# Kernel tuning notes

Measured on AMD Instinct MI355X. Metric: run time of the kernel, lower is better.

The kernel has to match this reference:

```python
import jax, jax.numpy as jnp
import numpy as np

NUM_HEADS = 8
DIM_V = 128
LN_EPS = 1e-5


def _ln(x, g, b):
    m = jnp.mean(x, axis=-1, keepdims=True)
    v = jnp.var(x, axis=-1, keepdims=True)
    return (x - m) * jax.lax.rsqrt(v + LN_EPS) * g + b


def _gcn(x, adj_norm, W, b):
    # DenseGCNConv: out = D^-1/2 (A+I) D^-1/2 (x W) + b
    return jnp.einsum('bnm,bmf->bnf', adj_norm, x @ W) + b


def setup_inputs() -> dict:
    key = jax.random.key(0)
    ks = jax.random.split(key, 24)
    B, N, D = 8, 1024, 128
    Hd = NUM_HEADS * DIM_V  # 1024
    s = lambda fan: 1.0 / np.sqrt(fan)
    inp = {
        'H': jax.random.normal(ks[0], (B, N, D), jnp.float32),
        'A': jax.random.uniform(ks[1], (B, N, N), jnp.float32),
        'W_Q': jax.random.normal(ks[2], (D, Hd), jnp.float32) * s(D),
        'b_Q': jnp.zeros((Hd,), jnp.float32),
        'W_K': jax.random.normal(ks[3], (D, Hd), jnp.float32) * s(D),
        'b_K': jnp.zeros((Hd,), jnp.float32),
        'W_V': jax.random.normal(ks[4], (D, Hd), jnp.float32) * s(D),
        'b_V': jnp.zeros((Hd,), jnp.float32),
        'B_bias': jax.random.normal(ks[5], (NUM_HEADS, N, N), jnp.float32) * 0.02,
        'W_O': jax.random.normal(ks[6], (Hd, D), jnp.float32) * s(Hd),
        'g0': jnp.ones((D,), jnp.float32), 'be0': jnp.zeros((D,), jnp.float32),
        'g1': jnp.ones((D,), jnp.float32), 'be1': jnp.zeros((D,), jnp.float32),
        'g2': jnp.ones((D,), jnp.float32), 'be2': jnp.zeros((D,), jnp.float32),
        'g3': jnp.ones((D,), jnp.float32), 'be3': jnp.zeros((D,), jnp.float32),
        'W1': jax.random.normal(ks[7], (D, D), jnp.float32) * s(D),
        'b1': jnp.zeros((D,), jnp.float32),
        'W2': jax.random.normal(ks[8], (D, D), jnp.float32) * s(D),
        'b2': jnp.zeros((D,), jnp.float32),
    }
    return inp


def reference(H, A, W_Q, b_Q, W_K, b_K, W_V, b_V, B_bias, W_O,
              g0, be0, g1, be1, g2, be2, g3, be3, W1, b1, W2, b2):
    B, N, D = H.shape
    dk_scale = 1.0 / np.sqrt(np.float32(D))  # sqrt(dim_K)

    residual = H
    Hn = _ln(H, g0, be0)  # norm_type 'sw': pre-norm

    # GCN adjacency normalization with self-loops (shared by Q/K/V layers)
    I = jnp.eye(N, dtype=A.dtype)
    Ahat = A * (1.0 - I) + I
    dis = jax.lax.rsqrt(jnp.maximum(Ahat.sum(-1), 1.0))  # [B,N]
    adj_norm = dis[:, :, None] * Ahat * dis[:, None, :]

    Q = _gcn(Hn, adj_norm, W_Q, b_Q)  # [B,N,H*dV]
    K = _gcn(Hn, adj_norm, W_K, b_K)
    V = _gcn(Hn, adj_norm, W_V, b_V)

    # split heads: feature slice h*dV:(h+1)*dV -> head h
    Q_ = Q.reshape(B, N, NUM_HEADS, DIM_V).transpose(0, 2, 1, 3)
    K_ = K.reshape(B, N, NUM_HEADS, DIM_V).transpose(0, 2, 1, 3)
    V_ = V.reshape(B, N, NUM_HEADS, DIM_V).transpose(0, 2, 1, 3)

    scores = jnp.einsum('bhnd,bhmd->bhnm', Q_, K_) * dk_scale
    scores = scores + B_bias[None]  # 'BL': blended with learned per-head bias
    attn = jax.nn.softmax(scores, axis=-1)
    MH = jnp.einsum('bhnm,bhmd->bhnd', attn, V_)  # [B,H,N,dV]

    MH = _ln(MH, g1, be1)  # 'sw' GN1

    # concat heads back to features
    MHc = MH.transpose(0, 2, 1, 3).reshape(B, N, NUM_HEADS * DIM_V)
    O = MHc @ W_O + residual
    O = _ln(O, g2, be2)

    RO = jax.nn.relu(jax.nn.relu(O @ W1 + b1) @ W2 + b2)
    RO = _ln(RO, g3, be3)  # 'sw' GN3
    return O + RO
```

## Files before the change

### kernel.cpp

```cpp
#include <hip/hip_runtime.h>
#include <hip/hip_bf16.h>
#include <stdint.h>

typedef __attribute__((ext_vector_type(8))) short bf16x8;
typedef __attribute__((ext_vector_type(4))) short s16x4;
typedef __attribute__((ext_vector_type(4))) float f32x4;

__device__ __forceinline__ float bf2f(short s) {
    union { float f; uint32_t u; } v; v.u = ((uint32_t)(uint16_t)s) << 16; return v.f;
}
__device__ __forceinline__ short f2bf(float f) {
    union { float f; uint32_t u; } v; v.f = f;
    uint32_t u = v.u;
    u += 0x7FFFu + ((u >> 16) & 1u);
    return (short)(u >> 16);
}
__device__ __forceinline__ void gload_lds16(const void* g, void* l) {
    __builtin_amdgcn_global_load_lds(
        (const __attribute__((address_space(1))) uint32_t*)g,
        (__attribute__((address_space(3))) uint32_t*)l, 16, 0, 0);
}

template<int MODE>
__global__ __launch_bounds__(256) void ln_kernel(
    const float* __restrict__ x, const float* __restrict__ res,
    const float* __restrict__ gamma, const float* __restrict__ beta,
    float* __restrict__ outf, short* __restrict__ outb)
{
    const int row = blockIdx.x * 4 + (threadIdx.x >> 6);
    const int lane = threadIdx.x & 63;
    const long base = (long)row * 128;
    float2 v;
    if (MODE == 1) {
        v.x = 0.f; v.y = 0.f;
#pragma unroll
        for (int p = 0; p < 2; ++p) {
            float2 t = *(const float2*)(x + (long)p * 1048576 + base + lane * 2);
            v.x += t.x; v.y += t.y;
        }
        float2 rr = *(const float2*)(res + base + lane * 2);
        v.x += rr.x; v.y += rr.y;
    } else {
        v = *(const float2*)(x + base + lane * 2);
    }
    float s = v.x + v.y, s2 = v.x * v.x + v.y * v.y;
#pragma unroll
    for (int o = 32; o; o >>= 1) { s += __shfl_xor(s, o); s2 += __shfl_xor(s2, o); }
    const float mean = s * (1.f / 128.f);
    const float var = s2 * (1.f / 128.f) - mean * mean;
    const float rs = rsqrtf(var + 1e-5f);
    const float y0 = (v.x - mean) * rs * gamma[lane * 2] + beta[lane * 2];
    const float y1 = (v.y - mean) * rs * gamma[lane * 2 + 1] + beta[lane * 2 + 1];
    if (MODE == 0 || MODE == 1) {
        uint32_t pk = (uint32_t)(uint16_t)f2bf(y0) | ((uint32_t)(uint16_t)f2bf(y1) << 16);
        *(uint32_t*)(outb + base + lane * 2) = pk;
    }
    if (MODE == 1) {
        float2 o2; o2.x = y0; o2.y = y1;
        *(float2*)(outf + base + lane * 2) = o2;
    }
    if (MODE == 2) {
        float2 rr = *(const float2*)(res + base + lane * 2);
        float2 o2; o2.x = y0 + rr.x; o2.y = y1 + rr.y;
        *(float2*)(outf + base + lane * 2) = o2;
    }
}

__global__ __launch_bounds__(256) void prep1_kernel(
    const float* __restrict__ H, const float* __restrict__ A, const float* __restrict__ Bb,
    const float* __restrict__ WQ, const float* __restrict__ WK, const float* __restrict__ WV,
    const float* __restrict__ bQ, const float* __restrict__ bK, const float* __restrict__ bV,
    const float* __restrict__ WO, const float* __restrict__ W1, const float* __restrict__ W2,
    const float* __restrict__ g0, const float* __restrict__ be0,
    short* __restrict__ Hn, float* __restrict__ dis, short* __restrict__ biasb,
    short* __restrict__ WqkvT, float* __restrict__ bqkv, short* __restrict__ WoT,
    short* __restrict__ W1T, short* __restrict__ W2T)
{
    __shared__ float red[4];
    const int id = blockIdx.x;
    const int tid = threadIdx.x;
    if (id < 2048) {
        const int row = id * 4 + (tid >> 6);
        const int lane = tid & 63;
        const long base = (long)row * 128;
        float2 v = *(const float2*)(H + base + lane * 2);
        float s = v.x + v.y, s2 = v.x * v.x + v.y * v.y;
#pragma unroll
        for (int o = 32; o; o >>= 1) { s += __shfl_xor(s, o); s2 += __shfl_xor(s2, o); }
        const float mean = s * (1.f / 128.f);
        const float var = s2 * (1.f / 128.f) - mean * mean;
        const float rs = rsqrtf(var + 1e-5f);
        const float y0 = (v.x - mean) * rs * g0[lane * 2] + be0[lane * 2];
        const float y1 = (v.y - mean) * rs * g0[lane * 2 + 1] + be0[lane * 2 + 1];
        uint32_t pk = (uint32_t)(uint16_t)f2bf(y0) | ((uint32_t)(uint16_t)f2bf(y1) << 16);
        *(uint32_t*)(Hn + base + lane * 2) = pk;
    } else if (id < 10240) {
        const int bn = id - 2048;
        const int n = bn & 1023;
        float4 v = ((const float4*)(A + (long)bn * 1024))[tid];
        float s = v.x + v.y + v.z + v.w;
        if ((n >> 2) == tid) {
            s += 1.f - ((const float*)&v)[n & 3];
        }
#pragma unroll
        for (int o = 32; o; o >>= 1) s += __shfl_xor(s, o);
        if ((tid & 63) == 0) red[tid >> 6] = s;
        __syncthreads();
        if (tid == 0) {
            float t = red[0] + red[1] + red[2] + red[3];
            dis[bn] = rsqrtf(fmaxf(t, 1.f));
        }
    } else if (id < 18432) {
        const long i = ((long)(id - 10240) * 256 + tid) * 4;
        float4 v = *(const float4*)(Bb + i);
        s16x4 o; o[0] = f2bf(v.x); o[1] = f2bf(v.y); o[2] = f2bf(v.z); o[3] = f2bf(v.w);
        *(s16x4*)(biasb + i) = o;
    } else {
        const int gid = (id - 18432) * 256 + tid;
        if (gid < 393216) {
            const int f = gid >> 7, k = gid & 127;
            const float* W = (f < 1024) ? WQ : (f < 2048 ? WK : WV);
            WqkvT[gid] = f2bf(W[k * 1024 + (f & 1023)]);
        } else if (gid < 396288) {
            const int f = gid - 393216;
            const float* bb = (f < 1024) ? bQ : (f < 2048 ? bK : bV);
            bqkv[f] = bb[f & 1023];
        } else if (gid < 527360) {
            const int t = gid - 396288;
            const int j = t >> 10, i = t & 1023;
            WoT[t] = f2bf(WO[i * 128 + j]);
        } else if (gid < 543744) {
            const int t = gid - 527360;
            W1T[t] = f2bf(W1[(t & 127) * 128 + (t >> 7)]);
        } else if (gid < 560128) {
            const int t = gid - 543744;
            W2T[t] = f2bf(W2[(t & 127) * 128 + (t >> 7)]);
        }
    }
}

__global__ __launch_bounds__(256) void prep2_kernel(
    const float* __restrict__ A, const float* __restrict__ dis, const short* __restrict__ Hn,
    short* __restrict__ adj, short* __restrict__ HnT)
{
    __shared__ short T[64][72];
    const int id = blockIdx.x;
    const int tid = threadIdx.x;
    if (id < 8192) {
        const int bn = id;
        const int b = bn >> 10, n = bn & 1023;
        const float dn = dis[bn];
        float4 v = ((const float4*)(A + (long)bn * 1024))[tid];
        const int m0 = tid * 4;
        const float* dm = dis + b * 1024 + m0;
        s16x4 o;
#pragma unroll
        for (int j = 0; j < 4; ++j) {
            float av = (m0 + j == n) ? 1.f : ((const float*)&v)[j];
            o[j] = f2bf(av * dn * dm[j]);
        }
        *(s16x4*)(adj + (long)bn * 1024 + m0) = o;
    } else {
        const int t = id - 8192;
        const int bx = t & 15, by = (t >> 4) & 1, bz = t >> 5;
        const int m0 = bx * 64, f0 = by * 64;
        const int row = tid >> 2;
        const int c = (tid & 3) * 16;
        const short* src = Hn + (long)(bz * 1024 + m0 + row) * 128 + f0 + c;
        *(bf16x8*)&T[row][c] = *(const bf16x8*)src;
        *(bf16x8*)&T[row][c + 8] = *(const bf16x8*)(src + 8);
        __syncthreads();
        short* dst = HnT + ((long)bz * 128 + f0 + row) * 1024 + m0 + c;
        bf16x8 o0, o1;
#pragma unroll
        for (int i = 0; i < 8; ++i) { o0[i] = T[c + i][row]; o1[i] = T[c + 8 + i][row]; }
        *(bf16x8*)dst = o0;
        *(bf16x8*)(dst + 8) = o1;
    }
}

__global__ __launch_bounds__(256) void ahred_kernel(const float* __restrict__ AHp, short* __restrict__ AH)
{
    const long i = ((long)blockIdx.x * 256 + threadIdx.x) * 4;
    const int b = (int)(i >> 17);
    const long r = i & 131071;
    const float* p = AHp + (long)b * 262144 + r;
    float4 v0 = *(const float4*)p;
    float4 v1 = *(const float4*)(p + 131072);
    s16x4 o;
    o[0] = f2bf(v0.x + v1.x);
    o[1] = f2bf(v0.y + v1.y);
    o[2] = f2bf(v0.z + v1.z);
    o[3] = f2bf(v0.w + v1.w);
    *(s16x4*)(AH + i) = o;
}

__global__ __launch_bounds__(256) void vtrans_kernel(const short* __restrict__ QKV, short* __restrict__ VT)
{
    const int bh = blockIdx.z, b = bh >> 3, h = bh & 7;
    const int n0 = blockIdx.x * 64, d0 = blockIdx.y * 64;
    __shared__ short T[64][72];
    const int row = threadIdx.x >> 2;
    const int c = (threadIdx.x & 3) * 16;
    const short* src = QKV + (long)(b * 1024 + n0 + row) * 3072 + 2048 + h * 128 + d0 + c;
    *(bf16x8*)&T[row][c] = *(const bf16x8*)src;
    *(bf16x8*)&T[row][c + 8] = *(const bf16x8*)(src + 8);
    __syncthreads();
    short* dst = VT + (long)(bh * 128 + d0 + row) * 1024 + n0 + c;
    bf16x8 o0, o1;
#pragma unroll
    for (int i = 0; i < 8; ++i) { o0[i] = T[c + i][row]; o1[i] = T[c + 8 + i][row]; }
    *(bf16x8*)dst = o0;
    *(bf16x8*)(dst + 8) = o1;
}

template<int BIAS_MODE, bool RELU, bool OUT_BF16>
__global__ __launch_bounds__(256) void gemm_kernel(
    const short* __restrict__ A, const short* __restrict__ Bt,
    const float* __restrict__ bias, void* __restrict__ Cv,
    int K, int lda, int ldb, int ldc,
    long batchA, long batchB, long batchC)
{
    __shared__ __align__(16) short Asm[128 * 32];
    __shared__ __align__(16) short Bsm[128 * 32];
    const int tid = threadIdx.x, lane = tid & 63, wave = tid >> 6;
    const int li = lane & 15, g = lane >> 4;
    const int mt = blockIdx.y * 128, nt = blockIdx.x * 128;
    A += (long)blockIdx.z * batchA;
    Bt += (long)blockIdx.z * batchB;

    const int wr = (wave >> 1) * 64, wc = (wave & 1) * 64;
    f32x4 acc[4][4] = {};

    const int srow = lane >> 2;
    const int scol = (lane & 3) * 8;
    const long aoff0 = (long)(mt + wave * 32 + srow) * lda + scol;
    const long aoff1 = aoff0 + (long)16 * lda;
    const long boff0 = (long)(nt + wave * 32 + srow) * ldb + scol;
    const long boff1 = boff0 + (long)16 * ldb;
    short* ad0 = &Asm[wave * 1024];
    short* ad1 = &Asm[wave * 1024 + 512];
    short* bd0 = &Bsm[wave * 1024];
    short* bd1 = &Bsm[wave * 1024 + 512];

    for (int k0 = 0; k0 < K; k0 += 32) {
        gload_lds16(A + aoff0 + k0, ad0);
        gload_lds16(A + aoff1 + k0, ad1);
        gload_lds16(Bt + boff0 + k0, bd0);
        gload_lds16(Bt + boff1 + k0, bd1);
        __syncthreads();
        bf16x8 af[4], bf[4];
#pragma unroll
        for (int m = 0; m < 4; ++m) af[m] = *(const bf16x8*)&Asm[(wr + m * 16 + li) * 32 + g * 8];
#pragma unroll
        for (int n = 0; n < 4; ++n) bf[n] = *(const bf16x8*)&Bsm[(wc + n * 16 + li) * 32 + g * 8];
#pragma unroll
        for (int m = 0; m < 4; ++m)
#pragma unroll
            for (int n = 0; n < 4; ++n)
                acc[m][n] = __builtin_amdgcn_mfma_f32_16x16x32_bf16(af[m], bf[n], acc[m][n], 0, 0, 0);
        __syncthreads();
    }

    const long cbase = (long)blockIdx.z * batchC;
#pragma unroll
    for (int m = 0; m < 4; ++m) {
        const int row0 = mt + wr + m * 16 + g * 4;
#pragma unroll
        for (int n = 0; n < 4; ++n) {
            const int col = nt + wc + n * 16 + li;
            float bc = (BIAS_MODE == 1) ? bias[col] : 0.f;
#pragma unroll
            for (int r = 0; r < 4; ++r) {
                float x = acc[m][n][r] + bc;
                if (RELU) x = fmaxf(x, 0.f);
                const long idx = cbase + (long)(row0 + r) * ldc + col;
                if (OUT_BF16) ((short*)Cv)[idx] = f2bf(x);
                else          ((float*)Cv)[idx] = x;
            }
        }
    }
}

template<int BIAS_MODE, bool RELU, bool OUT_BF16, int KSPLIT = 1>
__global__ __launch_bounds__(256) void gemm64_kernel(
    const short* __restrict__ A, const short* __restrict__ Bt,
    const float* __restrict__ bias, void* __restrict__ Cv,
    int K, int lda, int ldb, int ldc,
    long batchA, long batchB, long batchC)
{
    __shared__ __align__(16) short Asm[64 * 32];
    __shared__ __align__(16) short Bsm[64 * 32];
    const int tid = threadIdx.x, lane = tid & 63, wave = tid >> 6;
    const int li = lane & 15, g = lane >> 4;
    const int mt = blockIdx.y * 64, nt = blockIdx.x * 64;
    const int wr = (wave >> 1) * 32, wc = (wave & 1) * 32;
    const int zb = blockIdx.z / KSPLIT;
    const int kc = blockIdx.z % KSPLIT;
    A += (long)zb * batchA + (long)kc * K;
    Bt += (long)zb * batchB + (long)kc * K;
    f32x4 acc[2][2] = {};

    const int srow = lane >> 2;
    const int scol = (lane & 3) * 8;
    const long aoff = (long)(mt + wave * 16 + srow) * lda + scol;
    const long boff = (long)(nt + wave * 16 + srow) * ldb + scol;

    for (int k0 = 0; k0 < K; k0 += 32) {
        gload_lds16(A + aoff + k0, &Asm[wave * 512]);
        gload_lds16(Bt + boff + k0, &Bsm[wave * 512]);
        __syncthreads();
        bf16x8 af[2], bf[2];
#pragma unroll
        for (int m = 0; m < 2; ++m) af[m] = *(const bf16x8*)&Asm[(wr + m * 16 + li) * 32 + g * 8];
#pragma unroll
        for (int n = 0; n < 2; ++n) bf[n] = *(const bf16x8*)&Bsm[(wc + n * 16 + li) * 32 + g * 8];
#pragma unroll
        for (int m = 0; m < 2; ++m)
#pragma unroll
            for (int n = 0; n < 2; ++n)
                acc[m][n] = __builtin_amdgcn_mfma_f32_16x16x32_bf16(af[m], bf[n], acc[m][n], 0, 0, 0);
        __syncthreads();
    }

    const long cbase = (long)blockIdx.z * batchC;
#pragma unroll
    for (int m = 0; m < 2; ++m) {
        const int row0 = mt + wr + m * 16 + g * 4;
#pragma unroll
        for (int n = 0; n < 2; ++n) {
            const int col = nt + wc + n * 16 + li;
            float bc = (BIAS_MODE == 1) ? bias[col] : 0.f;
#pragma unroll
            for (int r = 0; r < 4; ++r) {
                float x = acc[m][n][r] + bc;
                if (RELU) x = fmaxf(x, 0.f);
                const long idx = cbase + (long)(row0 + r) * ldc + col;
                if (OUT_BF16) ((short*)Cv)[idx] = f2bf(x);
                else          ((float*)Cv)[idx] = x;
            }
        }
    }
}

__global__ __launch_bounds__(512, 2) void attn_kernel(
    const short* __restrict__ QKV, const short* __restrict__ VT,
    const short* __restrict__ biasb,
    const float* __restrict__ g1v, const float* __restrict__ be1v,
    short* __restrict__ MHc)
{
    const int tid = threadIdx.x;
    const int lane = tid & 63;
    const int wave = tid >> 6;
    const int li = lane & 15;
    const int g = lane >> 4;

    const int id = blockIdx.x;
    const int h = id & 7;
    const int b = (id >> 3) & 7;
    const int qt = id >> 6;
    const int q0 = qt * 128;

    __shared__ __align__(16) short Ksm[64 * 128];
    __shared__ __align__(16) short Vsm[128 * 64];
    __shared__ __align__(16) short Psm[8][16 * 72];

    bf16x8 qf[4];
    {
        const short* Qb = QKV + ((long)(b * 1024 + q0 + wave * 16 + li) * 3072 + h * 128);
#pragma unroll
        for (int dc = 0; dc < 4; ++dc)
            qf[dc] = *(const bf16x8*)(Qb + dc * 32 + g * 8);
    }

    float ll[4];
#pragma unroll
    for (int r = 0; r < 4; ++r) ll[r] = 0.f;
    f32x4 oacc[8] = {};

    const long kbase = (long)(b * 1024) * 3072 + 1024 + h * 128;
    const int kr0 = wave * 8 + g;
    const int kc0 = ((li * 16) ^ ((kr0 & 7) << 4)) >> 1;
    const int kc1 = ((li * 16) ^ (((kr0 + 4) & 7) << 4)) >> 1;
    const int vd_loc = lane >> 3;
    const int vcol = (((lane & 7) * 16) ^ (vd_loc << 4)) >> 1;
    const long vrowbase = ((long)(b * 8 + h) * 128) * 1024;

    const float scale = 0.08838834764831845f;
    const long bb_row0 = (long)h * 1024 + q0 + wave * 16 + g * 4;

    for (int kv0 = 0; kv0 < 1024; kv0 += 64) {
        gload_lds16(QKV + kbase + (long)(kv0 + kr0) * 3072 + kc0, &Ksm[wave * 1024]);
        gload_lds16(QKV + kbase + (long)(kv0 + kr0 + 4) * 3072 + kc1, &Ksm[wave * 1024 + 512]);
        gload_lds16(VT + vrowbase + (long)(wave * 16 + vd_loc) * 1024 + kv0 + vcol,
                    &Vsm[(wave * 16) * 64]);
        gload_lds16(VT + vrowbase + (long)(wave * 16 + 8 + vd_loc) * 1024 + kv0 + vcol,
                    &Vsm[(wave * 16 + 8) * 64]);
        __syncthreads();

        float bs[4][4];
#pragma unroll
        for (int r = 0; r < 4; ++r) {
            const short* bp = biasb + (bb_row0 + r) * 1024 + kv0 + li;
#pragma unroll
            for (int j = 0; j < 4; ++j)
                bs[r][j] = bf2f(bp[j * 16]);
        }

        const f32x4 fz = {0.f, 0.f, 0.f, 0.f};
        f32x4 sacc[4] = {fz, fz, fz, fz};
#pragma unroll
        for (int j = 0; j < 4; ++j) {
            const int r = j * 16 + li;
            const int sw = (r & 7) << 4;
#pragma unroll
            for (int dc = 0; dc < 4; ++dc) {
                bf16x8 kf = *(const bf16x8*)((const char*)Ksm + r * 256 + ((dc * 64 + g * 16) ^ sw));
                sacc[j] = __builtin_amdgcn_mfma_f32_16x16x32_bf16(qf[dc], kf, sacc[j], 0, 0, 0);
            }
        }

#pragma unroll
        for (int r = 0; r < 4; ++r) {
            short* pp = &Psm[wave][(g * 4 + r) * 72];
            float psum = 0.f;
#pragma unroll
            for (int j = 0; j < 4; ++j) {
                const float p = __expf(sacc[j][r] * scale + bs[r][j]);
                psum += p;
                pp[j * 16 + li] = f2bf(p);
            }
            ll[r] += psum;
        }

#pragma unroll
        for (int c = 0; c < 2; ++c) {
            bf16x8 pf = *(const bf16x8*)((const char*)&Psm[wave][0] + li * 144 + c * 64 + g * 16);
#pragma unroll
            for (int df = 0; df < 8; ++df) {
                bf16x8 vf = *(const bf16x8*)((const char*)Vsm + (df * 16 + li) * 128
                                             + ((c * 64 + g * 16) ^ ((li & 7) << 4)));
                oacc[df] = __builtin_amdgcn_mfma_f32_16x16x32_bf16(pf, vf, oacc[df], 0, 0, 0);
            }
        }
        __syncthreads();
    }

#pragma unroll
    for (int r = 0; r < 4; ++r) {
        const int qloc = g * 4 + r;
        float l = ll[r];
#pragma unroll
        for (int o = 1; o < 16; o <<= 1) l += __shfl_xor(l, o);
        const float inv = 1.f / l;
        float vals[8];
        float s1 = 0.f, s2 = 0.f;
#pragma unroll
        for (int df = 0; df < 8; ++df) {
            float v = oacc[df][r] * inv;
            vals[df] = v; s1 += v; s2 += v * v;
        }
#pragma unroll
        for (int o = 1; o < 16; o <<= 1) { s1 += __shfl_xor(s1, o); s2 += __shfl_xor(s2, o); }
        const float mean = s1 * (1.f / 128.f);
        const float var = s2 * (1.f / 128.f) - mean * mean;
        const float rs = rsqrtf(var + 1e-5f);
        const long orow = (long)(b * 1024 + q0 + wave * 16 + qloc) * 1024 + h * 128;
#pragma unroll
        for (int df = 0; df < 8; ++df) {
            const int d = df * 16 + li;
            MHc[orow + d] = f2bf((vals[df] - mean) * rs * g1v[d] + be1v[d]);
        }
    }
}

extern "C" void kernel_launch(void* const* d_in, const int* in_sizes, int n_in,
                              void* d_out, int out_size, void* d_ws, size_t ws_size,
                              hipStream_t stream)
{
    const float* H  = (const float*)d_in[0];
    const float* A  = (const float*)d_in[1];
    const float* WQ = (const float*)d_in[2];
    const float* bQ = (const float*)d_in[3];
    const float* WK = (const float*)d_in[4];
    const float* bK = (const float*)d_in[5];
    const float* WV = (const float*)d_in[6];
    const float* bV = (const float*)d_in[7];
    const float* Bb = (const float*)d_in[8];
    const float* WO = (const float*)d_in[9];
    const float* g0 = (const float*)d_in[10]; const float* be0 = (const float*)d_in[11];
    const float* g1 = (const float*)d_in[12]; const float* be1 = (const float*)d_in[13];
    const float* g2 = (const float*)d_in[14]; const float* be2 = (const float*)d_in[15];
    const float* g3 = (const float*)d_in[16]; const float* be3 = (const float*)d_in[17];
    const float* W1 = (const float*)d_in[18]; const float* b1 = (const float*)d_in[19];
    const float* W2 = (const float*)d_in[20]; const float* b2 = (const float*)d_in[21];
    float* out = (float*)d_out;

    char* ws = (char*)d_ws;
    short* Hn    = (short*)(ws + 0);
    short* adj   = (short*)(ws + 2097152);
    float* dis   = (float*)(ws + 18874368);
    short* WqkvT = (short*)(ws + 18907136);
    float* bqkv  = (float*)(ws + 19693568);
    short* WoT   = (short*)(ws + 19705856);
    short* W1T   = (short*)(ws + 19968000);
    short* W2T   = (short*)(ws + 20000768);
    short* biasb = (short*)(ws + 20033536);
    short* QKV   = (short*)(ws + 36810752);
    float* AHp   = (float*)(ws + 87142400);
    short* AH    = (short*)(ws + 103919616);
    short* HnT   = (short*)(ws + 106016768);
    short* VT    = adj;
    short* MHc   = (short*)(ws + 87142400);
    float* preO4 = (float*)(ws + 36810752);
    float* O     = (float*)(ws + 108113920);
    short* Obf   = (short*)(ws + 112308224);
    short* G1    = (short*)(ws + 114405376);
    float* G2    = (float*)(ws + 116502528);

    prep1_kernel<<<20620, 256, 0, stream>>>(H, A, Bb, WQ, WK, WV, bQ, bK, bV,
                                            WO, W1, W2, g0, be0,
                                            Hn, dis, biasb, WqkvT, bqkv, WoT, W1T, W2T);
    prep2_kernel<<<8448, 256, 0, stream>>>(A, dis, Hn, adj, HnT);

    gemm64_kernel<0, false, false, 2><<<dim3(2, 16, 16), 256, 0, stream>>>(
        adj, HnT, nullptr, AHp, 512, 1024, 1024, 128,
        1048576L, 131072L, 131072L);
    ahred_kernel<<<1024, 256, 0, stream>>>(AHp, AH);

    gemm_kernel<1, false, true><<<dim3(24, 64, 1), 256, 0, stream>>>(
        AH, WqkvT, bqkv, QKV, 128, 128, 128, 3072, 0, 0, 0);

    vtrans_kernel<<<dim3(16, 2, 64), 256, 0, stream>>>(QKV, VT);
    attn_kernel<<<512, 512, 0, stream>>>(QKV, VT, biasb, g1, be1, MHc);

    gemm64_kernel<0, false, false, 2><<<dim3(2, 128, 2), 256, 0, stream>>>(
        MHc, WoT, nullptr, preO4, 512, 1024, 1024, 128, 0, 0, 1048576L);
    ln_kernel<1><<<2048, 256, 0, stream>>>(preO4, H, g2, be2, O, Obf);
    gemm64_kernel<1, true, true><<<dim3(2, 128, 1), 256, 0, stream>>>(
        Obf, W1T, b1, G1, 128, 128, 128, 128, 0, 0, 0);
    gemm64_kernel<1, true, false><<<dim3(2, 128, 1), 256, 0, stream>>>(
        G1, W2T, b2, G2, 128, 128, 128, 128, 0, 0, 0);
    ln_kernel<2><<<2048, 256, 0, stream>>>(G2, O, g3, be3, out, nullptr);
}
```

Before: 163.6 us.

## Split attention over two KV halves with separate combine and LayerNorm kernel

The attention kernel now runs on a 2-D grid where each block handles half of the key/value range. Each block writes unnormalized partial outputs in bf16 plus its partial softmax denominators. A new combine kernel sums the two partials, normalizes them and applies the GN1 LayerNorm. The bias is also prescaled by log2(e) during prep, so the inner loop can use exp2f with a folded scale instead of __expf. The split is meant to double the number of attention blocks for better CU occupancy and tail balance, at the cost of extra partial-output traffic and an additional kernel launch.

After: 184.7 us. 1.13x slower.

```diff
diff --git a/kernel.cpp b/kernel.cpp
--- a/kernel.cpp
+++ b/kernel.cpp
@@ -51,11 +51,9 @@
     const float rs = rsqrtf(var + 1e-5f);
     const float y0 = (v.x - mean) * rs * gamma[lane * 2] + beta[lane * 2];
     const float y1 = (v.y - mean) * rs * gamma[lane * 2 + 1] + beta[lane * 2 + 1];
-    if (MODE == 0 || MODE == 1) {
+    if (MODE == 1) {
         uint32_t pk = (uint32_t)(uint16_t)f2bf(y0) | ((uint32_t)(uint16_t)f2bf(y1) << 16);
         *(uint32_t*)(outb + base + lane * 2) = pk;
-    }
-    if (MODE == 1) {
         float2 o2; o2.x = y0; o2.y = y1;
         *(float2*)(outf + base + lane * 2) = o2;
     }
@@ -111,9 +109,11 @@
             dis[bn] = rsqrtf(fmaxf(t, 1.f));
         }
     } else if (id < 18432) {
+        const float l2e = 1.4426950408889634f;
         const long i = ((long)(id - 10240) * 256 + tid) * 4;
         float4 v = *(const float4*)(Bb + i);
-        s16x4 o; o[0] = f2bf(v.x); o[1] = f2bf(v.y); o[2] = f2bf(v.z); o[3] = f2bf(v.w);
+        s16x4 o; o[0] = f2bf(v.x * l2e); o[1] = f2bf(v.y * l2e);
+        o[2] = f2bf(v.z * l2e); o[3] = f2bf(v.w * l2e);
         *(s16x4*)(biasb + i) = o;
     } else {
         const int gid = (id - 18432) * 256 + tid;
@@ -346,8 +346,7 @@
 __global__ __launch_bounds__(512, 2) void attn_kernel(
     const short* __restrict__ QKV, const short* __restrict__ VT,
     const short* __restrict__ biasb,
-    const float* __restrict__ g1v, const float* __restrict__ be1v,
-    short* __restrict__ MHc)
+    short* __restrict__ Opart, float* __restrict__ llpart)
 {
     const int tid = threadIdx.x;
     const int lane = tid & 63;
@@ -360,6 +359,8 @@
     const int b = (id >> 3) & 7;
     const int qt = id >> 6;
     const int q0 = qt * 128;
+    const int kvh = blockIdx.y;
+    const int kvbeg = kvh << 9;
 
     __shared__ __align__(16) short Ksm[64 * 128];
     __shared__ __align__(16) short Vsm[128 * 64];
@@ -386,10 +387,10 @@
     const int vcol = (((lane & 7) * 16) ^ (vd_loc << 4)) >> 1;
     const long vrowbase = ((long)(b * 8 + h) * 128) * 1024;
 
-    const float scale = 0.08838834764831845f;
+    const float scale2 = 0.12753102f;
     const long bb_row0 = (long)h * 1024 + q0 + wave * 16 + g * 4;
 
-    for (int kv0 = 0; kv0 < 1024; kv0 += 64) {
+    for (int kv0 = kvbeg; kv0 < kvbeg + 512; kv0 += 64) {
         gload_lds16(QKV + kbase + (long)(kv0 + kr0) * 3072 + kc0, &Ksm[wave * 1024]);
         gload_lds16(QKV + kbase + (long)(kv0 + kr0 + 4) * 3072 + kc1, &Ksm[wave * 1024 + 512]);
         gload_lds16(VT + vrowbase + (long)(wave * 16 + vd_loc) * 1024 + kv0 + vcol,
@@ -426,7 +427,7 @@
             float psum = 0.f;
 #pragma unroll
             for (int j = 0; j < 4; ++j) {
-                const float p = __expf(sacc[j][r] * scale + bs[r][j]);
+                const float p = exp2f(sacc[j][r] * scale2 + bs[r][j]);
                 psum += p;
                 pp[j * 16 + li] = f2bf(p);
             }
@@ -452,26 +453,47 @@
         float l = ll[r];
 #pragma unroll
         for (int o = 1; o < 16; o <<= 1) l += __shfl_xor(l, o);
-        const float inv = 1.f / l;
-        float vals[8];
-        float s1 = 0.f, s2 = 0.f;
-#pragma unroll
-        for (int df = 0; df < 8; ++df) {
-            float v = oacc[df][r] * inv;
-            vals[df] = v; s1 += v; s2 += v * v;
-        }
-#pragma unroll
-        for (int o = 1; o < 16; o <<= 1) { s1 += __shfl_xor(s1, o); s2 += __shfl_xor(s2, o); }
-        const float mean = s1 * (1.f / 128.f);
-        const float var = s2 * (1.f / 128.f) - mean * mean;
-        const float rs = rsqrtf(var + 1e-5f);
-        const long orow = (long)(b * 1024 + q0 + wave * 16 + qloc) * 1024 + h * 128;
-#pragma unroll
-        for (int df = 0; df < 8; ++df) {
-            const int d = df * 16 + li;
-            MHc[orow + d] = f2bf((vals[df] - mean) * rs * g1v[d] + be1v[d]);
-        }
-    }
+        const int q = q0 + wave * 16 + qloc;
+        if (li == 0)
+            llpart[((long)(kvh * 8 + b) * 8 + h) * 1024 + q] = l;
+        const long orow = (long)kvh * 8388608 + (long)(b * 1024 + q) * 1024 + h * 128;
+#pragma unroll
+        for (int df = 0; df < 8; ++df)
+            Opart[orow + df * 16 + li] = f2bf(oacc[df][r]);
+    }
+}
+
+__global__ __launch_bounds__(256) void attncomb_kernel(
+    const short* __restrict__ Opart, const float* __restrict__ llpart,
+    const float* __restrict__ g1v, const float* __restrict__ be1v,
+    short* __restrict__ MHc)
+{
+    const int unit = blockIdx.x * 4 + (threadIdx.x >> 6);
+    const int lane = threadIdx.x & 63;
+    const int h = unit & 7;
+    const int rowg = unit >> 3;
+    const int b = rowg >> 10;
+    const long lidx = ((long)b * 8 + h) * 1024 + (rowg & 1023);
+    const float l = llpart[lidx] + llpart[65536 + lidx];
+    const float inv = 1.f / l;
+
+    const long base = (long)rowg * 1024 + h * 128 + lane * 2;
+    uint32_t u0 = *(const uint32_t*)(Opart + base);
+    uint32_t u1 = *(const uint32_t*)(Opart + 8388608 + base);
+    const float x0 = (bf2f((short)(u0 & 0xFFFF)) + bf2f((short)(u1 & 0xFFFF))) * inv;
+    const float x1 = (bf2f((short)(u0 >> 16)) + bf2f((short)(u1 >> 16))) * inv;
+
+    float s = x0 + x1, s2 = x0 * x0 + x1 * x1;
+#pragma unroll
+    for (int o = 32; o; o >>= 1) { s += __shfl_xor(s, o); s2 += __shfl_xor(s2, o); }
+    const float mean = s * (1.f / 128.f);
+    const float var = s2 * (1.f / 128.f) - mean * mean;
+    const float rs = rsqrtf(var + 1e-5f);
+    const int d = lane * 2;
+    const float y0 = (x0 - mean) * rs * g1v[d] + be1v[d];
+    const float y1 = (x1 - mean) * rs * g1v[d + 1] + be1v[d + 1];
+    uint32_t pk = (uint32_t)(uint16_t)f2bf(y0) | ((uint32_t)(uint16_t)f2bf(y1) << 16);
+    *(uint32_t*)(MHc + base) = pk;
 }
 
 extern "C" void kernel_launch(void* const* d_in, const int* in_sizes, int n_in,
@@ -511,7 +533,9 @@
     short* AH    = (short*)(ws + 103919616);
     short* HnT   = (short*)(ws + 106016768);
     short* VT    = adj;
-    short* MHc   = (short*)(ws + 87142400);
+    short* Opart = (short*)(ws + 87142400);
+    float* llpart= (float*)(ws + 18874368);
+    short* MHc   = (short*)(ws + 2097152);
     float* preO4 = (float*)(ws + 36810752);
     float* O     = (float*)(ws + 108113920);
     short* Obf   = (short*)(ws + 112308224);
@@ -532,7 +556,9 @@
         AH, WqkvT, bqkv, QKV, 128, 128, 128, 3072, 0, 0, 0);
 
     vtrans_kernel<<<dim3(16, 2, 64), 256, 0, stream>>>(QKV, VT);
-    attn_kernel<<<512, 512, 0, stream>>>(QKV, VT, biasb, g1, be1, MHc);
+
+    attn_kernel<<<dim3(512, 2), 512, 0, stream>>>(QKV, VT, biasb, Opart, llpart);
+    attncomb_kernel<<<16384, 256, 0, stream>>>(Opart, llpart, g1, be1, MHc);
 
     gemm64_kernel<0, false, false, 2><<<dim3(2, 128, 2), 256, 0, stream>>>(
         MHc, WoT, nullptr, preO4, 512, 1024, 1024, 128, 0, 0, 1048576L);
```

## Fuse V transpose into QKV GEMM epilogue and switch softmax to exp2

Applied to the files above, without the earlier changes.

The QKV projection GEMM now writes the V columns straight into the transposed per-head VT layout in its epilogue, which removes the separate vtrans kernel launch and its extra read and write of V. The attention softmax uses exp2f with a log2(e)-folded scale, and the bf16 bias is prescaled by log2(e) in prep, which saves a multiply per exponent. The epilogue for V now does strided 8-byte stores instead of coalesced row stores. The unused MODE 0 path in the LayerNorm kernel is also trimmed.

Result: slower. 175.6 us (+7.3%).

```diff
diff --git a/kernel.cpp b/kernel.cpp
--- a/kernel.cpp
+++ b/kernel.cpp
@@ -51,11 +51,9 @@
     const float rs = rsqrtf(var + 1e-5f);
     const float y0 = (v.x - mean) * rs * gamma[lane * 2] + beta[lane * 2];
     const float y1 = (v.y - mean) * rs * gamma[lane * 2 + 1] + beta[lane * 2 + 1];
-    if (MODE == 0 || MODE == 1) {
+    if (MODE == 1) {
         uint32_t pk = (uint32_t)(uint16_t)f2bf(y0) | ((uint32_t)(uint16_t)f2bf(y1) << 16);
         *(uint32_t*)(outb + base + lane * 2) = pk;
-    }
-    if (MODE == 1) {
         float2 o2; o2.x = y0; o2.y = y1;
         *(float2*)(outf + base + lane * 2) = o2;
     }
@@ -111,9 +109,11 @@
             dis[bn] = rsqrtf(fmaxf(t, 1.f));
         }
     } else if (id < 18432) {
+        const float l2e = 1.4426950408889634f;
         const long i = ((long)(id - 10240) * 256 + tid) * 4;
         float4 v = *(const float4*)(Bb + i);
-        s16x4 o; o[0] = f2bf(v.x); o[1] = f2bf(v.y); o[2] = f2bf(v.z); o[3] = f2bf(v.w);
+        s16x4 o; o[0] = f2bf(v.x * l2e); o[1] = f2bf(v.y * l2e);
+        o[2] = f2bf(v.z * l2e); o[3] = f2bf(v.w * l2e);
         *(s16x4*)(biasb + i) = o;
     } else {
         const int gid = (id - 18432) * 256 + tid;
@@ -195,31 +195,12 @@
     *(s16x4*)(AH + i) = o;
 }
 
-__global__ __launch_bounds__(256) void vtrans_kernel(const short* __restrict__ QKV, short* __restrict__ VT)
-{
-    const int bh = blockIdx.z, b = bh >> 3, h = bh & 7;
-    const int n0 = blockIdx.x * 64, d0 = blockIdx.y * 64;
-    __shared__ short T[64][72];
-    const int row = threadIdx.x >> 2;
-    const int c = (threadIdx.x & 3) * 16;
-    const short* src = QKV + (long)(b * 1024 + n0 + row) * 3072 + 2048 + h * 128 + d0 + c;
-    *(bf16x8*)&T[row][c] = *(const bf16x8*)src;
-    *(bf16x8*)&T[row][c + 8] = *(const bf16x8*)(src + 8);
-    __syncthreads();
-    short* dst = VT + (long)(bh * 128 + d0 + row) * 1024 + n0 + c;
-    bf16x8 o0, o1;
-#pragma unroll
-    for (int i = 0; i < 8; ++i) { o0[i] = T[c + i][row]; o1[i] = T[c + 8 + i][row]; }
-    *(bf16x8*)dst = o0;
-    *(bf16x8*)(dst + 8) = o1;
-}
-
-template<int BIAS_MODE, bool RELU, bool OUT_BF16>
+template<int BIAS_MODE, bool RELU, bool OUT_BF16, bool VTOUT = false>
 __global__ __launch_bounds__(256) void gemm_kernel(
     const short* __restrict__ A, const short* __restrict__ Bt,
     const float* __restrict__ bias, void* __restrict__ Cv,
     int K, int lda, int ldb, int ldc,
-    long batchA, long batchB, long batchC)
+    long batchA, long batchB, long batchC, short* __restrict__ VTp = nullptr)
 {
     __shared__ __align__(16) short Asm[128 * 32];
     __shared__ __align__(16) short Bsm[128 * 32];
@@ -270,13 +251,26 @@
         for (int n = 0; n < 4; ++n) {
             const int col = nt + wc + n * 16 + li;
             float bc = (BIAS_MODE == 1) ? bias[col] : 0.f;
-#pragma unroll
-            for (int r = 0; r < 4; ++r) {
-                float x = acc[m][n][r] + bc;
-                if (RELU) x = fmaxf(x, 0.f);
-                const long idx = cbase + (long)(row0 + r) * ldc + col;
-                if (OUT_BF16) ((short*)Cv)[idx] = f2bf(x);
-                else          ((float*)Cv)[idx] = x;
+            if (VTOUT && col >= 2048) {
+                const int d = col & 127;
+                const int h = (col >> 7) & 7;
+                s16x4 o4;
+#pragma unroll
+                for (int r = 0; r < 4; ++r) {
+                    float x = acc[m][n][r] + bc;
+                    o4[r] = f2bf(x);
+                }
+                short* dst = VTp + ((long)((row0 >> 10) * 8 + h) * 128 + d) * 1024 + (row0 & 1023);
+                *(s16x4*)dst = o4;
+            } else {
+#pragma unroll
+                for (int r = 0; r < 4; ++r) {
+                    float x = acc[m][n][r] + bc;
+                    if (RELU) x = fmaxf(x, 0.f);
+                    const long idx = cbase + (long)(row0 + r) * ldc + col;
+                    if (OUT_BF16) ((short*)Cv)[idx] = f2bf(x);
+                    else          ((float*)Cv)[idx] = x;
+                }
             }
         }
     }
@@ -386,7 +380,7 @@
     const int vcol = (((lane & 7) * 16) ^ (vd_loc << 4)) >> 1;
     const long vrowbase = ((long)(b * 8 + h) * 128) * 1024;
 
-    const float scale = 0.08838834764831845f;
+    const float scale2 = 0.12753102f;
     const long bb_row0 = (long)h * 1024 + q0 + wave * 16 + g * 4;
 
     for (int kv0 = 0; kv0 < 1024; kv0 += 64) {
@@ -426,7 +420,7 @@
             float psum = 0.f;
 #pragma unroll
             for (int j = 0; j < 4; ++j) {
-                const float p = __expf(sacc[j][r] * scale + bs[r][j]);
+                const float p = exp2f(sacc[j][r] * scale2 + bs[r][j]);
                 psum += p;
                 pp[j * 16 + li] = f2bf(p);
             }
@@ -528,10 +522,9 @@
         1048576L, 131072L, 131072L);
     ahred_kernel<<<1024, 256, 0, stream>>>(AHp, AH);
 
-    gemm_kernel<1, false, true><<<dim3(24, 64, 1), 256, 0, stream>>>(
-        AH, WqkvT, bqkv, QKV, 128, 128, 128, 3072, 0, 0, 0);
-
-    vtrans_kernel<<<dim3(16, 2, 64), 256, 0, stream>>>(QKV, VT);
+    gemm_kernel<1, false, true, true><<<dim3(24, 64, 1), 256, 0, stream>>>(
+        AH, WqkvT, bqkv, QKV, 128, 128, 128, 3072, 0, 0, 0, VT);
+
     attn_kernel<<<512, 512, 0, stream>>>(QKV, VT, biasb, g1, be1, MHc);
 
     gemm64_kernel<0, false, false, 2><<<dim3(2, 128, 2), 256, 0, stream>>>(
```

## Fuse adjacency normalization into the A·Hn GEMM and drop the bf16 adj buffer

Applied to the files above, without the earlier changes.

Instead of writing a normalized bf16 adjacency matrix (16 MB) in prep2 and reading it back in a generic GEMM, a new ahgemm kernel loads raw fp32 A, applies the self-loop and D^-1/2 scaling in registers, converts to bf16 and stores it to LDS before the MFMA. This removes one full write and one full read of the adjacency. In exchange, the fp32 A read doubles the A-side bytes per tile, and the new kernel is single-buffered with a synchronous register load path, so latency hiding may be worse than in the previous GEMM. The MODE==0 LN branch is also trimmed.

After: 171.6 us, median of 2. 1.05x slower.

```diff
diff --git a/kernel.cpp b/kernel.cpp
--- a/kernel.cpp
+++ b/kernel.cpp
@@ -51,11 +51,9 @@
     const float rs = rsqrtf(var + 1e-5f);
     const float y0 = (v.x - mean) * rs * gamma[lane * 2] + beta[lane * 2];
     const float y1 = (v.y - mean) * rs * gamma[lane * 2 + 1] + beta[lane * 2 + 1];
-    if (MODE == 0 || MODE == 1) {
+    if (MODE == 1) {
         uint32_t pk = (uint32_t)(uint16_t)f2bf(y0) | ((uint32_t)(uint16_t)f2bf(y1) << 16);
         *(uint32_t*)(outb + base + lane * 2) = pk;
-    }
-    if (MODE == 1) {
         float2 o2; o2.x = y0; o2.y = y1;
         *(float2*)(outf + base + lane * 2) = o2;
     }
@@ -139,43 +137,94 @@
     }
 }
 
-__global__ __launch_bounds__(256) void prep2_kernel(
-    const float* __restrict__ A, const float* __restrict__ dis, const short* __restrict__ Hn,
-    short* __restrict__ adj, short* __restrict__ HnT)
+__global__ __launch_bounds__(256) void prep2_kernel(const short* __restrict__ Hn, short* __restrict__ HnT)
 {
     __shared__ short T[64][72];
     const int id = blockIdx.x;
     const int tid = threadIdx.x;
-    if (id < 8192) {
-        const int bn = id;
-        const int b = bn >> 10, n = bn & 1023;
-        const float dn = dis[bn];
-        float4 v = ((const float4*)(A + (long)bn * 1024))[tid];
-        const int m0 = tid * 4;
-        const float* dm = dis + b * 1024 + m0;
-        s16x4 o;
+    const int bx = id & 15, by = (id >> 4) & 1, bz = id >> 5;
+    const int m0 = bx * 64, f0 = by * 64;
+    const int row = tid >> 2;
+    const int c = (tid & 3) * 16;
+    const short* src = Hn + (long)(bz * 1024 + m0 + row) * 128 + f0 + c;
+    *(bf16x8*)&T[row][c] = *(const bf16x8*)src;
+    *(bf16x8*)&T[row][c + 8] = *(const bf16x8*)(src + 8);
+    __syncthreads();
+    short* dst = HnT + ((long)bz * 128 + f0 + row) * 1024 + m0 + c;
+    bf16x8 o0, o1;
+#pragma unroll
+    for (int i = 0; i < 8; ++i) { o0[i] = T[c + i][row]; o1[i] = T[c + 8 + i][row]; }
+    *(bf16x8*)dst = o0;
+    *(bf16x8*)(dst + 8) = o1;
+}
+
+__global__ __launch_bounds__(256) void ahgemm_kernel(
+    const float* __restrict__ A, const float* __restrict__ dis,
+    const short* __restrict__ HnT, float* __restrict__ AHp)
+{
+    __shared__ __align__(16) short Asm[64 * 32];
+    __shared__ __align__(16) short Bsm[64 * 32];
+    const int tid = threadIdx.x, lane = tid & 63, wave = tid >> 6;
+    const int li = lane & 15, g = lane >> 4;
+    const int mt = blockIdx.y * 64, nt = blockIdx.x * 64;
+    const int wr = (wave >> 1) * 32, wc = (wave & 1) * 32;
+    const int zb = blockIdx.z >> 1;
+    const int kc = blockIdx.z & 1;
+    f32x4 acc[2][2] = {};
+
+    const int srow = lane >> 2;
+    const int scol = (lane & 3) * 8;
+    const int grow = mt + wave * 16 + srow;
+    const float dn = dis[zb * 1024 + grow];
+    const float* Ab = A + (long)zb * 1048576 + (long)grow * 1024 + kc * 512 + scol;
+    const float* db = dis + zb * 1024 + kc * 512 + scol;
+    const short* Bg = HnT + (long)zb * 131072 + (long)(nt + wave * 16 + srow) * 1024 + kc * 512 + scol;
+    short* ad = &Asm[(wave * 16 + srow) * 32 + scol];
+
+    for (int k0 = 0; k0 < 512; k0 += 32) {
+        gload_lds16(Bg + k0, &Bsm[wave * 512]);
+        float4 a0 = *(const float4*)(Ab + k0);
+        float4 a1 = *(const float4*)(Ab + k0 + 4);
+        float4 d0 = *(const float4*)(db + k0);
+        float4 d1 = *(const float4*)(db + k0 + 4);
+        const int col0 = kc * 512 + k0 + scol;
+        bf16x8 o;
 #pragma unroll
         for (int j = 0; j < 4; ++j) {
-            float av = (m0 + j == n) ? 1.f : ((const float*)&v)[j];
-            o[j] = f2bf(av * dn * dm[j]);
-        }
-        *(s16x4*)(adj + (long)bn * 1024 + m0) = o;
-    } else {
-        const int t = id - 8192;
-        const int bx = t & 15, by = (t >> 4) & 1, bz = t >> 5;
-        const int m0 = bx * 64, f0 = by * 64;
-        const int row = tid >> 2;
-        const int c = (tid & 3) * 16;
-        const short* src = Hn + (long)(bz * 1024 + m0 + row) * 128 + f0 + c;
-        *(bf16x8*)&T[row][c] = *(const bf16x8*)src;
-        *(bf16x8*)&T[row][c + 8] = *(const bf16x8*)(src + 8);
-        __syncthreads();
-        short* dst = HnT + ((long)bz * 128 + f0 + row) * 1024 + m0 + c;
-        bf16x8 o0, o1;
-#pragma unroll
-        for (int i = 0; i < 8; ++i) { o0[i] = T[c + i][row]; o1[i] = T[c + 8 + i][row]; }
-        *(bf16x8*)dst = o0;
-        *(bf16x8*)(dst + 8) = o1;
+            float av = (grow == col0 + j) ? 1.f : ((const float*)&a0)[j];
+            o[j] = f2bf(av * dn * ((const float*)&d0)[j]);
+        }
+#pragma unroll
+        for (int j = 0; j < 4; ++j) {
+            float av = (grow == col0 + 4 + j) ? 1.f : ((const float*)&a1)[j];
+            o[4 + j] = f2bf(av * dn * ((const float*)&d1)[j]);
+        }
+        *(bf16x8*)ad = o;
+        __syncthreads();
+        bf16x8 af[2], bf[2];
+#pragma unroll
+        for (int m = 0; m < 2; ++m) af[m] = *(const bf16x8*)&Asm[(wr + m * 16 + li) * 32 + g * 8];
+#pragma unroll
+        for (int n = 0; n < 2; ++n) bf[n] = *(const bf16x8*)&Bsm[(wc + n * 16 + li) * 32 + g * 8];
+#pragma unroll
+        for (int m = 0; m < 2; ++m)
+#pragma unroll
+            for (int n = 0; n < 2; ++n)
+                acc[m][n] = __builtin_amdgcn_mfma_f32_16x16x32_bf16(af[m], bf[n], acc[m][n], 0, 0, 0);
+        __syncthreads();
+    }
+
+    const long cbase = (long)blockIdx.z * 131072;
+#pragma unroll
+    for (int m = 0; m < 2; ++m) {
+        const int row0 = mt + wr + m * 16 + g * 4;
+#pragma unroll
+        for (int n = 0; n < 2; ++n) {
+            const int col = nt + wc + n * 16 + li;
+#pragma unroll
+            for (int r = 0; r < 4; ++r)
+                AHp[cbase + (long)(row0 + r) * 128 + col] = acc[m][n][r];
+        }
     }
 }
 
@@ -498,7 +547,7 @@
 
     char* ws = (char*)d_ws;
     short* Hn    = (short*)(ws + 0);
-    short* adj   = (short*)(ws + 2097152);
+    short* VT    = (short*)(ws + 2097152);
     float* dis   = (float*)(ws + 18874368);
     short* WqkvT = (short*)(ws + 18907136);
     float* bqkv  = (float*)(ws + 19693568);
@@ -510,7 +559,6 @@
     float* AHp   = (float*)(ws + 87142400);
     short* AH    = (short*)(ws + 103919616);
     short* HnT   = (short*)(ws + 106016768);
-    short* VT    = adj;
     short* MHc   = (short*)(ws + 87142400);
     float* preO4 = (float*)(ws + 36810752);
     float* O     = (float*)(ws + 108113920);
@@ -521,17 +569,16 @@
     prep1_kernel<<<20620, 256, 0, stream>>>(H, A, Bb, WQ, WK, WV, bQ, bK, bV,
                                             WO, W1, W2, g0, be0,
                                             Hn, dis, biasb, WqkvT, bqkv, WoT, W1T, W2T);
-    prep2_kernel<<<8448, 256, 0, stream>>>(A, dis, Hn, adj, HnT);
-
-    gemm64_kernel<0, false, false, 2><<<dim3(2, 16, 16), 256, 0, stream>>>(
-        adj, HnT, nullptr, AHp, 512, 1024, 1024, 128,
-        1048576L, 131072L, 131072L);
+    prep2_kernel<<<256, 256, 0, stream>>>(Hn, HnT);
+
+    ahgemm_kernel<<<dim3(2, 16, 16), 256, 0, stream>>>(A, dis, HnT, AHp);
     ahred_kernel<<<1024, 256, 0, stream>>>(AHp, AH);
 
     gemm_kernel<1, false, true><<<dim3(24, 64, 1), 256, 0, stream>>>(
         AH, WqkvT, bqkv, QKV, 128, 128, 128, 3072, 0, 0, 0);
 
     vtrans_kernel<<<dim3(16, 2, 64), 256, 0, stream>>>(QKV, VT);
+
     attn_kernel<<<512, 512, 0, stream>>>(QKV, VT, biasb, g1, be1, MHc);
 
     gemm64_kernel<0, false, false, 2><<<dim3(2, 128, 2), 256, 0, stream>>>(
```
